# Optimization experiments

Hardware: AMD Instinct MI355X
Metric: run time of the kernel (lower is better)

The kernel has to match this reference:

```python
import jax, jax.numpy as jnp
import numpy as np

B, C, T = 32, 128, 8192
K, M, G = 5, 2, 2          # ksize, fc1 expansion, fc2 groups multiplier
PAD = (K - 1) // 2
OUT_PER_GROUP = (C * C * K) // (G * C)   # fc2: groups=G*C, 1 in-ch per group


def setup_inputs() -> dict:
    key = jax.random.key(0)
    k1, k2, k3, k4 = jax.random.split(key, 4)
    x = jax.random.normal(k1, (B, C, T), dtype=jnp.float32)
    # valid lengths in [T//2, T] to avoid divide-by-zero in the masked GAP
    input_lengths = jax.random.randint(k2, (B,), T // 2, T + 1)
    # wn_fc1: Conv1d(C, M*C, 1) with bias -> weight (M*C, C), bias (M*C,)
    w1 = jax.random.normal(k3, (M * C, C), dtype=jnp.float32) * 0.02
    b1 = jnp.zeros((M * C,), dtype=jnp.float32)
    # wn_fc2: Conv1d(M*C, C*C*K, 1, groups=G*C, bias=False)
    # in/group = 1, so weight is effectively (C*C*K,) scalars
    w2 = jax.random.normal(k4, (C * C * K,), dtype=jnp.float32) * 0.02
    return {"x": x, "input_lengths": input_lengths, "w1": w1, "b1": b1, "w2": w2}


def _forward(x, input_lengths, w1, b1, w2):
    Bs, Cs, Ts = x.shape
    # global average pool over time, normalized by true lengths: (B, C)
    gap = x.sum(axis=2) / input_lengths[:, None].astype(x.dtype)
    # wn_fc1 (1x1 conv == dense) + sigmoid: (B, M*C)
    h = jax.nn.sigmoid(gap @ w1.T + b1)
    # wn_fc2 grouped 1x1 conv: group g reads channel g, writes OUT_PER_GROUP chans
    w2g = w2.reshape(M * Cs, OUT_PER_GROUP)              # (2C, C*K/2)
    flat = (h[:, :, None] * w2g[None]).reshape(Bs, -1)   # (B, C*C*K), group-major
    # per-sample conv weights, as in weight.view(B*oup, inp, ksize)
    w_dyn = flat.reshape(Bs * Cs, Cs, K)
    # conv1d_sample_by_sample: grouped conv with groups = B over (1, B*C, T)
    out = jax.lax.conv_general_dilated(
        x.reshape(1, Bs * Cs, Ts),
        w_dyn,
        window_strides=(1,),
        padding=[(PAD, PAD)],
        feature_group_count=Bs,
        dimension_numbers=("NCH", "OIH", "NCH"),
    )
    return out.reshape(Bs, Cs, Ts)


def reference(x, input_lengths, w1, b1, w2):
    return _forward(x, input_lengths, w1, b1, w2)
```

## Files before the change

kernel.cpp:

```cpp
#include <hip/hip_runtime.h>
#include <hip/hip_bf16.h>

#define B_  32
#define C_  128
#define T_  8192
#define K_  5
#define MC  256
#define WPB 81920

typedef short bf16x8 __attribute__((ext_vector_type(8)));
typedef float f32x4  __attribute__((ext_vector_type(4)));

static __device__ __forceinline__ unsigned short f2bf(float f) {
    unsigned int u = __float_as_uint(f);
    u += 0x7FFFu + ((u >> 16) & 1u);
    return (unsigned short)(u >> 16);
}

__global__ __launch_bounds__(256) void gap_kernel(const float* __restrict__ x,
                                                  const int* __restrict__ len,
                                                  float* __restrict__ gap) {
    const int row = blockIdx.x;
    const float* xr = x + (size_t)row * T_;
    const int tid = threadIdx.x;
    float s = 0.f;
    const float4* xv = reinterpret_cast<const float4*>(xr);
#pragma unroll
    for (int i = 0; i < T_ / 4 / 256; ++i) {
        float4 v = xv[tid + i * 256];
        s += v.x + v.y + v.z + v.w;
    }
#pragma unroll
    for (int off = 32; off; off >>= 1) s += __shfl_down(s, off);
    __shared__ float red[4];
    if ((tid & 63) == 0) red[tid >> 6] = s;
    __syncthreads();
    if (tid == 0) {
        float tot = red[0] + red[1] + red[2] + red[3];
        gap[row] = tot / (float)len[row >> 7];
    }
}

__global__ __launch_bounds__(256) void fc1_kernel(const float* __restrict__ gap,
                                                  const float* __restrict__ w1,
                                                  const float* __restrict__ b1,
                                                  float* __restrict__ h) {
    const int b = blockIdx.x;
    const int o = threadIdx.x;
    __shared__ float g[C_];
    if (o < C_) g[o] = gap[b * C_ + o];
    __syncthreads();
    float acc = b1[o];
    const float* wr = w1 + o * C_;
#pragma unroll 8
    for (int c = 0; c < C_; ++c) acc += g[c] * wr[c];
    h[b * MC + o] = 1.f / (1.f + expf(-acc));
}

__global__ __launch_bounds__(256) void wgen_kernel(const float* __restrict__ h,
                                                   const float* __restrict__ w2,
                                                   unsigned short* __restrict__ W) {
    const int idx = blockIdx.x * 256 + threadIdx.x;
    const int ci = idx & 127;
    const int t1 = idx >> 7;
    const int k  = t1 % 5;
    const int t2 = t1 / 5;
    const int co = t2 & 127;
    const int b  = t2 >> 7;
    const float hv = h[b * MC + 2 * co + (ci >= 64)];
    const float wv = w2[co * 640 + ci * 5 + k];
    W[idx] = f2bf(hv * wv);
}

__global__ __launch_bounds__(256) void conv_kernel(const float* __restrict__ x,
                                                   const unsigned short* __restrict__ W,
                                                   float* __restrict__ out) {
    const int t0 = blockIdx.x * 128;
    const int b  = blockIdx.y;
    const int tid = threadIdx.x;

    __shared__ unsigned short xs[136 * 136];

    const float* xb = x + (size_t)b * C_ * T_;
#pragma unroll
    for (int it = 0; it < 17; ++it) {
        int i  = tid + it * 256;
        int cg = i / 136;
        int tl = i - cg * 136;
        int t  = t0 - 4 + tl;
        float v0 = 0.f, v1 = 0.f, v2 = 0.f, v3 = 0.f;
        if (t >= 0 && t < T_) {
            const float* p = xb + (size_t)(4 * cg) * T_ + t;
            v0 = p[0]; v1 = p[T_]; v2 = p[2 * T_]; v3 = p[3 * T_];
        }
        ushort4 pk;
        pk.x = f2bf(v0); pk.y = f2bf(v1); pk.z = f2bf(v2); pk.w = f2bf(v3);
        *reinterpret_cast<ushort4*>(&xs[tl * 136 + 4 * cg]) = pk;
    }
    __syncthreads();

    const int w  = tid >> 6;
    const int l  = tid & 63;
    const int wr = w >> 1, wc = w & 1;
    const int lr = l & 15, lh = l >> 4;

    f32x4 acc[4][4];
#pragma unroll
    for (int mt = 0; mt < 4; ++mt)
#pragma unroll
        for (int nt = 0; nt < 4; ++nt)
#pragma unroll
            for (int r = 0; r < 4; ++r) acc[mt][nt][r] = 0.f;

    const unsigned short* Wb = W + (size_t)b * WPB;

#pragma unroll
    for (int k = 0; k < K_; ++k) {
#pragma unroll
        for (int kc = 0; kc < 4; ++kc) {
            bf16x8 Af[4], Bf[4];
#pragma unroll
            for (int mt = 0; mt < 4; ++mt) {
                int co = wr * 64 + mt * 16 + lr;
                Af[mt] = *reinterpret_cast<const bf16x8*>(
                    Wb + co * 640 + k * 128 + kc * 32 + 8 * lh);
            }
#pragma unroll
            for (int nt = 0; nt < 4; ++nt) {
                int row = wc * 64 + nt * 16 + lr + k + 2;
                Bf[nt] = *reinterpret_cast<const bf16x8*>(
                    &xs[row * 136 + kc * 32 + 8 * lh]);
            }
#pragma unroll
            for (int mt = 0; mt < 4; ++mt)
#pragma unroll
                for (int nt = 0; nt < 4; ++nt)
                    acc[mt][nt] = __builtin_amdgcn_mfma_f32_16x16x32_bf16(
                        Af[mt], Bf[nt], acc[mt][nt], 0, 0, 0);
        }
    }

    float* ob = out + (size_t)b * C_ * T_;
#pragma unroll
    for (int mt = 0; mt < 4; ++mt) {
#pragma unroll
        for (int nt = 0; nt < 4; ++nt) {
            int tcol = t0 + wc * 64 + nt * 16 + lr;
#pragma unroll
            for (int r = 0; r < 4; ++r) {
                int co = wr * 64 + mt * 16 + lh * 4 + r;
                ob[(size_t)co * T_ + tcol] = acc[mt][nt][r];
            }
        }
    }
}

extern "C" void kernel_launch(void* const* d_in, const int* in_sizes, int n_in,
                              void* d_out, int out_size, void* d_ws, size_t ws_size,
                              hipStream_t stream) {
    const float* x   = (const float*)d_in[0];
    const int*   len = (const int*)d_in[1];
    const float* w1  = (const float*)d_in[2];
    const float* b1  = (const float*)d_in[3];
    const float* w2  = (const float*)d_in[4];
    float* out = (float*)d_out;

    char* ws = (char*)d_ws;
    float* gap = (float*)ws;
    float* h   = (float*)(ws + 16384);
    unsigned short* W = (unsigned short*)(ws + 65536);

    gap_kernel<<<B_ * C_, 256, 0, stream>>>(x, len, gap);
    fc1_kernel<<<B_, 256, 0, stream>>>(gap, w1, b1, h);
    wgen_kernel<<<(B_ * WPB) / 256, 256, 0, stream>>>(h, w2, W);
    dim3 g(T_ / 128, B_);
    conv_kernel<<<g, 256, 0, stream>>>(x, W, out);
}
```

Measured before the change: 327.9 us.

## Fuse GAP with bf16 transpose of x and load conv tiles via direct LDS loads

```diff
diff --git a/kernel.cpp b/kernel.cpp
--- a/kernel.cpp
+++ b/kernel.cpp
@@ -7,6 +7,7 @@
 #define K_  5
 #define MC  256
 #define WPB 81920
+#define XT_ROWS 8208
 
 typedef short bf16x8 __attribute__((ext_vector_type(8)));
 typedef float f32x4  __attribute__((ext_vector_type(4)));
@@ -16,6 +17,136 @@
     u += 0x7FFFu + ((u >> 16) & 1u);
     return (unsigned short)(u >> 16);
 }
+
+static __device__ __forceinline__ void gload_lds16(const void* g, void* l) {
+    __builtin_amdgcn_global_load_lds(
+        (const __attribute__((address_space(1))) unsigned int*)g,
+        (__attribute__((address_space(3))) unsigned int*)l, 16, 0, 0);
+}
+
+
+__global__ __launch_bounds__(256) void zero_gap(float* __restrict__ gap) {
+    gap[blockIdx.x * 256 + threadIdx.x] = 0.f;
+}
+
+__global__ __launch_bounds__(256) void zero_pads(unsigned short* __restrict__ xT) {
+    const int b = blockIdx.x;
+    const int r = threadIdx.x >> 4, c = threadIdx.x & 15;
+    const int R = (r < 4) ? r : (8196 + r - 4);
+    bf16x8 z = {0, 0, 0, 0, 0, 0, 0, 0};
+    *(bf16x8*)((char*)(xT + (size_t)b * (XT_ROWS * 128)) + (size_t)R * 256 + 16 * c) = z;
+}
+
+__global__ __launch_bounds__(256) void tgap_kernel(const float* __restrict__ x,
+                                                   unsigned short* __restrict__ xT,
+                                                   float* __restrict__ gap) {
+    const int t0 = blockIdx.x * 64;
+    const int b  = blockIdx.y;
+    const int tid = threadIdx.x;
+    const int ci = tid >> 1;
+    const int half = tid & 1;
+
+    __shared__ unsigned short lt[64 * 128];
+
+    const float* xr = x + ((size_t)b * C_ + ci) * T_ + t0 + half * 32;
+    float s = 0.f;
+#pragma unroll
+    for (int j = 0; j < 8; ++j) {
+        float4 v = reinterpret_cast<const float4*>(xr)[j];
+        s += v.x + v.y + v.z + v.w;
+        int tt = half * 32 + j * 4;
+        lt[(tt + 0) * 128 + ci] = f2bf(v.x);
+        lt[(tt + 1) * 128 + ci] = f2bf(v.y);
+        lt[(tt + 2) * 128 + ci] = f2bf(v.z);
+        lt[(tt + 3) * 128 + ci] = f2bf(v.w);
+    }
+    s += __shfl_down(s, 1);
+    if (!half) atomicAdd(&gap[b * C_ + ci], s);
+    __syncthreads();
+
+    char* xTb = (char*)(xT + (size_t)b * (XT_ROWS * 128));
+#pragma unroll
+    for (int qq = 0; qq < 4; ++qq) {
+        int q = qq * 256 + tid;
+        int r = q >> 4, c = q & 15;
+        int R = t0 + 4 + r;
+        bf16x8 v = *reinterpret_cast<const bf16x8*>(&lt[r * 128 + c * 8]);
+        *reinterpret_cast<bf16x8*>(xTb + (size_t)R * 256 + 16 * (c ^ (R & 15))) = v;
+    }
+}
+
+__global__ __launch_bounds__(256, 4) void conv_fast(const unsigned short* __restrict__ xT,
+                                                    const unsigned short* __restrict__ W,
+                                                    float* __restrict__ out) {
+    const int t0 = blockIdx.x * 128;
+    const int b  = blockIdx.y;
+    const int tid = threadIdx.x;
+    const int w = tid >> 6, l = tid & 63;
+
+    __shared__ unsigned short xs[136 * 128];
+
+    const char* gbase = (const char*)(xT + (size_t)b * (XT_ROWS * 128))
+                        + (size_t)t0 * 256 + l * 16;
+    for (int j = w; j < 34; j += 4)
+        gload_lds16(gbase + j * 1024, (char*)xs + j * 1024);
+    __syncthreads();
+
+    const int wr = w >> 1, wc = w & 1;
+    const int lr = l & 15, lh = l >> 4;
+
+    f32x4 acc[4][4];
+#pragma unroll
+    for (int mt = 0; mt < 4; ++mt)
+#pragma unroll
+        for (int nt = 0; nt < 4; ++nt)
+#pragma unroll
+            for (int r = 0; r < 4; ++r) acc[mt][nt][r] = 0.f;
+
+    const unsigned short* Wb = W + (size_t)b * WPB;
+
+#pragma unroll
+    for (int k = 0; k < K_; ++k) {
+#pragma unroll
+        for (int kc = 0; kc < 4; ++kc) {
+            bf16x8 Af[4], Bf[4];
+#pragma unroll
+            for (int mt = 0; mt < 4; ++mt) {
+                int co = wr * 64 + mt * 16 + lr;
+                Af[mt] = *reinterpret_cast<const bf16x8*>(
+                    Wb + co * 640 + k * 128 + kc * 32 + 8 * lh);
+            }
+#pragma unroll
+            for (int nt = 0; nt < 4; ++nt) {
+                int row = wc * 64 + nt * 16 + lr + k + 2;
+                int c   = 4 * kc + lh;
+                int cs  = c ^ (row & 15);
+                Bf[nt] = *reinterpret_cast<const bf16x8*>(
+                    (const char*)xs + row * 256 + cs * 16);
+            }
+#pragma unroll
+            for (int mt = 0; mt < 4; ++mt)
+#pragma unroll
+                for (int nt = 0; nt < 4; ++nt)
+                    acc[mt][nt] = __builtin_amdgcn_mfma_f32_16x16x32_bf16(
+                        Af[mt], Bf[nt], acc[mt][nt], 0, 0, 0);
+        }
+    }
+
+    float* ob = out + (size_t)b * C_ * T_;
+#pragma unroll
+    for (int mt = 0; mt < 4; ++mt) {
+#pragma unroll
+        for (int nt = 0; nt < 4; ++nt) {
+            int tcol = t0 + wc * 64 + nt * 16 + lr;
+#pragma unroll
+            for (int r = 0; r < 4; ++r) {
+                int co = wr * 64 + mt * 16 + lh * 4 + r;
+                ob[(size_t)co * T_ + tcol] = acc[mt][nt][r];
+            }
+        }
+    }
+}
+
 
 __global__ __launch_bounds__(256) void gap_kernel(const float* __restrict__ x,
                                                   const int* __restrict__ len,
@@ -41,14 +172,97 @@
     }
 }
 
+__global__ __launch_bounds__(256) void conv_kernel(const float* __restrict__ x,
+                                                   const unsigned short* __restrict__ W,
+                                                   float* __restrict__ out) {
+    const int t0 = blockIdx.x * 128;
+    const int b  = blockIdx.y;
+    const int tid = threadIdx.x;
+    __shared__ unsigned short xs[136 * 136];
+    const float* xb = x + (size_t)b * C_ * T_;
+#pragma unroll
+    for (int it = 0; it < 17; ++it) {
+        int i  = tid + it * 256;
+        int cg = i / 136;
+        int tl = i - cg * 136;
+        int t  = t0 - 4 + tl;
+        float v0 = 0.f, v1 = 0.f, v2 = 0.f, v3 = 0.f;
+        if (t >= 0 && t < T_) {
+            const float* p = xb + (size_t)(4 * cg) * T_ + t;
+            v0 = p[0]; v1 = p[T_]; v2 = p[2 * T_]; v3 = p[3 * T_];
+        }
+        ushort4 pk;
+        pk.x = f2bf(v0); pk.y = f2bf(v1); pk.z = f2bf(v2); pk.w = f2bf(v3);
+        *reinterpret_cast<ushort4*>(&xs[tl * 136 + 4 * cg]) = pk;
+    }
+    __syncthreads();
+    const int w  = tid >> 6;
+    const int l  = tid & 63;
+    const int wr = w >> 1, wc = w & 1;
+    const int lr = l & 15, lh = l >> 4;
+    f32x4 acc[4][4];
+#pragma unroll
+    for (int mt = 0; mt < 4; ++mt)
+#pragma unroll
+        for (int nt = 0; nt < 4; ++nt)
+#pragma unroll
+            for (int r = 0; r < 4; ++r) acc[mt][nt][r] = 0.f;
+    const unsigned short* Wb = W + (size_t)b * WPB;
+#pragma unroll
+    for (int k = 0; k < K_; ++k) {
+#pragma unroll
+        for (int kc = 0; kc < 4; ++kc) {
+            bf16x8 Af[4], Bf[4];
+#pragma unroll
+            for (int mt = 0; mt < 4; ++mt) {
+                int co = wr * 64 + mt * 16 + lr;
+                Af[mt] = *reinterpret_cast<const bf16x8*>(
+                    Wb + co * 640 + k * 128 + kc * 32 + 8 * lh);
+            }
+#pragma unroll
+            for (int nt = 0; nt < 4; ++nt) {
+                int row = wc * 64 + nt * 16 + lr + k + 2;
+                Bf[nt] = *reinterpret_cast<const bf16x8*>(
+                    &xs[row * 136 + kc * 32 + 8 * lh]);
+            }
+#pragma unroll
+            for (int mt = 0; mt < 4; ++mt)
+#pragma unroll
+                for (int nt = 0; nt < 4; ++nt)
+                    acc[mt][nt] = __builtin_amdgcn_mfma_f32_16x16x32_bf16(
+                        Af[mt], Bf[nt], acc[mt][nt], 0, 0, 0);
+        }
+    }
+    float* ob = out + (size_t)b * C_ * T_;
+#pragma unroll
+    for (int mt = 0; mt < 4; ++mt) {
+#pragma unroll
+        for (int nt = 0; nt < 4; ++nt) {
+            int tcol = t0 + wc * 64 + nt * 16 + lr;
+#pragma unroll
+            for (int r = 0; r < 4; ++r) {
+                int co = wr * 64 + mt * 16 + lh * 4 + r;
+                ob[(size_t)co * T_ + tcol] = acc[mt][nt][r];
+            }
+        }
+    }
+}
+
+
 __global__ __launch_bounds__(256) void fc1_kernel(const float* __restrict__ gap,
+                                                  const int* __restrict__ len,
                                                   const float* __restrict__ w1,
                                                   const float* __restrict__ b1,
-                                                  float* __restrict__ h) {
+                                                  float* __restrict__ h,
+                                                  int divide) {
     const int b = blockIdx.x;
     const int o = threadIdx.x;
     __shared__ float g[C_];
-    if (o < C_) g[o] = gap[b * C_ + o];
+    if (o < C_) {
+        float v = gap[b * C_ + o];
+        if (divide) v /= (float)len[b];
+        g[o] = v;
+    }
     __syncthreads();
     float acc = b1[o];
     const float* wr = w1 + o * C_;
@@ -72,89 +286,6 @@
     W[idx] = f2bf(hv * wv);
 }
 
-__global__ __launch_bounds__(256) void conv_kernel(const float* __restrict__ x,
-                                                   const unsigned short* __restrict__ W,
-                                                   float* __restrict__ out) {
-    const int t0 = blockIdx.x * 128;
-    const int b  = blockIdx.y;
-    const int tid = threadIdx.x;
-
-    __shared__ unsigned short xs[136 * 136];
-
-    const float* xb = x + (size_t)b * C_ * T_;
-#pragma unroll
-    for (int it = 0; it < 17; ++it) {
-        int i  = tid + it * 256;
-        int cg = i / 136;
-        int tl = i - cg * 136;
-        int t  = t0 - 4 + tl;
-        float v0 = 0.f, v1 = 0.f, v2 = 0.f, v3 = 0.f;
-        if (t >= 0 && t < T_) {
-            const float* p = xb + (size_t)(4 * cg) * T_ + t;
-            v0 = p[0]; v1 = p[T_]; v2 = p[2 * T_]; v3 = p[3 * T_];
-        }
-        ushort4 pk;
-        pk.x = f2bf(v0); pk.y = f2bf(v1); pk.z = f2bf(v2); pk.w = f2bf(v3);
-        *reinterpret_cast<ushort4*>(&xs[tl * 136 + 4 * cg]) = pk;
-    }
-    __syncthreads();
-
-    const int w  = tid >> 6;
-    const int l  = tid & 63;
-    const int wr = w >> 1, wc = w & 1;
-    const int lr = l & 15, lh = l >> 4;
-
-    f32x4 acc[4][4];
-#pragma unroll
-    for (int mt = 0; mt < 4; ++mt)
-#pragma unroll
-        for (int nt = 0; nt < 4; ++nt)
-#pragma unroll
-            for (int r = 0; r < 4; ++r) acc[mt][nt][r] = 0.f;
-
-    const unsigned short* Wb = W + (size_t)b * WPB;
-
-#pragma unroll
-    for (int k = 0; k < K_; ++k) {
-#pragma unroll
-        for (int kc = 0; kc < 4; ++kc) {
-            bf16x8 Af[4], Bf[4];
-#pragma unroll
-            for (int mt = 0; mt < 4; ++mt) {
-                int co = wr * 64 + mt * 16 + lr;
-                Af[mt] = *reinterpret_cast<const bf16x8*>(
-                    Wb + co * 640 + k * 128 + kc * 32 + 8 * lh);
-            }
-#pragma unroll
-            for (int nt = 0; nt < 4; ++nt) {
-                int row = wc * 64 + nt * 16 + lr + k + 2;
-                Bf[nt] = *reinterpret_cast<const bf16x8*>(
-                    &xs[row * 136 + kc * 32 + 8 * lh]);
-            }
-#pragma unroll
-            for (int mt = 0; mt < 4; ++mt)
-#pragma unroll
-                for (int nt = 0; nt < 4; ++nt)
-                    acc[mt][nt] = __builtin_amdgcn_mfma_f32_16x16x32_bf16(
-                        Af[mt], Bf[nt], acc[mt][nt], 0, 0, 0);
-        }
-    }
-
-    float* ob = out + (size_t)b * C_ * T_;
-#pragma unroll
-    for (int mt = 0; mt < 4; ++mt) {
-#pragma unroll
-        for (int nt = 0; nt < 4; ++nt) {
-            int tcol = t0 + wc * 64 + nt * 16 + lr;
-#pragma unroll
-            for (int r = 0; r < 4; ++r) {
-                int co = wr * 64 + mt * 16 + lh * 4 + r;
-                ob[(size_t)co * T_ + tcol] = acc[mt][nt][r];
-            }
-        }
-    }
-}
-
 extern "C" void kernel_launch(void* const* d_in, const int* in_sizes, int n_in,
                               void* d_out, int out_size, void* d_ws, size_t ws_size,
                               hipStream_t stream) {
@@ -169,10 +300,24 @@
     float* gap = (float*)ws;
     float* h   = (float*)(ws + 16384);
     unsigned short* W = (unsigned short*)(ws + 65536);
-
-    gap_kernel<<<B_ * C_, 256, 0, stream>>>(x, len, gap);
-    fc1_kernel<<<B_, 256, 0, stream>>>(gap, w1, b1, h);
-    wgen_kernel<<<(B_ * WPB) / 256, 256, 0, stream>>>(h, w2, W);
-    dim3 g(T_ / 128, B_);
-    conv_kernel<<<g, 256, 0, stream>>>(x, W, out);
-}
+    unsigned short* xT = (unsigned short*)(ws + 65536 + (size_t)B_ * WPB * 2);
+    const size_t need = 65536 + (size_t)B_ * WPB * 2
+                      + (size_t)B_ * XT_ROWS * C_ * 2;
+
+    if (ws_size >= need) {
+        zero_gap<<<B_ * C_ / 256, 256, 0, stream>>>(gap);
+        zero_pads<<<B_, 256, 0, stream>>>(xT);
+        dim3 gt(T_ / 64, B_);
+        tgap_kernel<<<gt, 256, 0, stream>>>(x, xT, gap);
+        fc1_kernel<<<B_, 256, 0, stream>>>(gap, len, w1, b1, h, 1);
+        wgen_kernel<<<(B_ * WPB) / 256, 256, 0, stream>>>(h, w2, W);
+        dim3 g(T_ / 128, B_);
+        conv_fast<<<g, 256, 0, stream>>>(xT, W, out);
+    } else {
+        gap_kernel<<<B_ * C_, 256, 0, stream>>>(x, len, gap);
+        fc1_kernel<<<B_, 256, 0, stream>>>(gap, len, w1, b1, h, 0);
+        wgen_kernel<<<(B_ * WPB) / 256, 256, 0, stream>>>(h, w2, W);
+        dim3 g(T_ / 128, B_);
+        conv_kernel<<<g, 256, 0, stream>>>(x, W, out);
+    }
+}
```

Result: slower. 338.8 us (+3.3%).
